# Optimization experiments

Measured on AMD Instinct MI355X. Metric: run time of the kernel, lower is better.

Reference implementation:

```python
import jax, jax.numpy as jnp
import numpy as np

SMOOTH = 1.0

def reference(probs, targets):
    B = probs.shape[0]
    m1 = probs.reshape(B, -1)
    m2 = targets.reshape(B, -1)
    # thresholded prediction and per-sample argmax ground truth (original acc branch)
    SR = m1 > 0.5
    GT = m2 == jnp.max(m2, axis=1, keepdims=True)
    corr = jnp.sum(SR == GT, axis=1).astype(jnp.float32)
    # original divides by SR.shape[0] == probs.shape[1] (per-sample first dim)
    acc = corr / jnp.float32(probs.shape[1])
    intersection = jnp.sum(m1 * m2, axis=1)
    score = 2.0 * (intersection + SMOOTH) / (jnp.sum(m1, axis=1) + jnp.sum(m2, axis=1) + SMOOTH)
    score = jnp.where(acc == 1.0, jnp.float32(1.0), score)
    return jnp.mean(1.0 - score)

def setup_inputs() -> dict:
    key = jax.random.key(0)
    k1, k2 = jax.random.split(key)
    probs = jax.random.uniform(k1, (32, 1, 512, 512), dtype=jnp.float32)
    targets = jax.random.uniform(k2, (32, 1, 512, 512), dtype=jnp.float32)
    return {"probs": probs, "targets": targets}
```

## Files before the change

kernel.cpp:

```cpp
#include <hip/hip_runtime.h>
#include <math.h>

#define NS 32
#define NELEM 262144
#define TPB 256

__device__ __forceinline__ unsigned f2u(float x) { return __builtin_bit_cast(unsigned, x); }
__device__ __forceinline__ float u2f(unsigned x) { return __builtin_bit_cast(float, x); }

__device__ __forceinline__ void comb(float& mx, int& pk, float m2, int pk2) {
    const bool g = m2 > mx;
    const bool e = m2 == mx;
    pk = g ? pk2 : (pk + (e ? pk2 : 0));
    mx = fmaxf(mx, m2);
}

template<int CTRL>
__device__ __forceinline__ float dppf(float v) {
    return u2f((unsigned)__builtin_amdgcn_update_dpp((int)f2u(v), (int)f2u(v),
                                                     CTRL, 0xF, 0xF, false));
}
template<int CTRL>
__device__ __forceinline__ int dppi(int v) {
    return __builtin_amdgcn_update_dpp(v, v, CTRL, 0xF, 0xF, false);
}

template<int N>
__device__ __forceinline__ void level_ror(float& s1, float& s2, float& dt,
                                          int& cgt, float& mx, int& pk) {
    s1 += dppf<0x120 + N>(s1);
    s2 += dppf<0x120 + N>(s2);
    dt += dppf<0x120 + N>(dt);
    cgt += dppi<0x120 + N>(cgt);
    const float m2 = dppf<0x120 + N>(mx);
    const int   p2 = dppi<0x120 + N>(pk);
    comb(mx, pk, m2, p2);
}

#if __has_builtin(__builtin_amdgcn_permlane16_swap) && __has_builtin(__builtin_amdgcn_permlane32_swap)
template<bool WIDE>
__device__ __forceinline__ void level_swap(float& s1, float& s2, float& dt,
                                           int& cgt, float& mx, int& pk) {
#define SWAP_(x) (WIDE ? __builtin_amdgcn_permlane32_swap((x), (x), false, false) \
                       : __builtin_amdgcn_permlane16_swap((x), (x), false, false))
    { auto r = SWAP_(f2u(s1)); s1 = u2f(r[0]) + u2f(r[1]); }
    { auto r = SWAP_(f2u(s2)); s2 = u2f(r[0]) + u2f(r[1]); }
    { auto r = SWAP_(f2u(dt)); dt = u2f(r[0]) + u2f(r[1]); }
    { auto r = SWAP_((unsigned)cgt); cgt = (int)(r[0] + r[1]); }
    { auto rm = SWAP_(f2u(mx));
      auto rp = SWAP_((unsigned)pk);
      float mA = u2f(rm[0]); int pA = (int)rp[0];
      comb(mA, pA, u2f(rm[1]), (int)rp[1]);
      mx = mA; pk = pA; }
#undef SWAP_
}
#else
template<bool WIDE>
__device__ __forceinline__ void level_swap(float& s1, float& s2, float& dt,
                                           int& cgt, float& mx, int& pk) {
    const int off = WIDE ? 32 : 16;
    s1 += __shfl_xor(s1, off);
    s2 += __shfl_xor(s2, off);
    dt += __shfl_xor(dt, off);
    cgt += __shfl_xor(cgt, off);
    const float m2 = __shfl_xor(mx, off);
    const int   p2 = __shfl_xor(pk, off);
    comb(mx, pk, m2, p2);
}
#endif

template<int PASSES, int MINW>
__global__ __launch_bounds__(TPB, MINW) void k_partial(const float* __restrict__ probs,
                                                       const float* __restrict__ tgts,
                                                       float* __restrict__ wsf,
                                                       int* __restrict__ wsi,
                                                       int nsets) {
    constexpr int BPS = NELEM / (PASSES * TPB * 16);
    const int b = blockIdx.x;
    const int s = b / BPS;
    const int c = b % BPS;
    const size_t base = (size_t)s * NELEM + (size_t)c * (PASSES * TPB * 16);
    const float4* __restrict__ p4 = (const float4*)(probs + base);
    const float4* __restrict__ t4 = (const float4*)(tgts + base);
    const int t = threadIdx.x;

    float4 a1 = {0.f,0.f,0.f,0.f}, a2 = {0.f,0.f,0.f,0.f}, ad = {0.f,0.f,0.f,0.f};
    int cgt = 0, pk = 0;
    float mx = -INFINITY;

#pragma unroll
    for (int g = 0; g < PASSES; ++g) {
        float4 pv[4], tv[4];
#pragma unroll
        for (int k = 0; k < 4; ++k) {
            pv[k] = p4[g * 1024 + k * 256 + t];
            tv[k] = t4[g * 1024 + k * 256 + t];
        }
#pragma unroll
        for (int k = 0; k < 4; ++k) {
            a1.x += pv[k].x; a1.y += pv[k].y; a1.z += pv[k].z; a1.w += pv[k].w;
            a2.x += tv[k].x; a2.y += tv[k].y; a2.z += tv[k].z; a2.w += tv[k].w;
            ad.x = fmaf(pv[k].x, tv[k].x, ad.x);
            ad.y = fmaf(pv[k].y, tv[k].y, ad.y);
            ad.z = fmaf(pv[k].z, tv[k].z, ad.z);
            ad.w = fmaf(pv[k].w, tv[k].w, ad.w);
        }
        const float mX = fmaxf(fmaxf(tv[0].x, tv[1].x), fmaxf(tv[2].x, tv[3].x));
        const float mY = fmaxf(fmaxf(tv[0].y, tv[1].y), fmaxf(tv[2].y, tv[3].y));
        const float mZ = fmaxf(fmaxf(tv[0].z, tv[1].z), fmaxf(tv[2].z, tv[3].z));
        const float mW = fmaxf(fmaxf(tv[0].w, tv[1].w), fmaxf(tv[2].w, tv[3].w));
        const float mg = fmaxf(fmaxf(mX, mY), fmaxf(mZ, mW));
        int cp = 0, cg = 0, gg = 0;
#pragma unroll
        for (int k = 0; k < 4; ++k) {
            const float pc[4] = {pv[k].x, pv[k].y, pv[k].z, pv[k].w};
            const float tc[4] = {tv[k].x, tv[k].y, tv[k].z, tv[k].w};
#pragma unroll
            for (int j = 0; j < 4; ++j) {
                const int b1 = pc[j] > 0.5f;
                const int eq = tc[j] == mg;
                cp += b1;
                cg += eq;
                gg += eq & b1;
            }
        }
        cgt += cp;
        comb(mx, pk, mg, (cg << 16) | gg);
    }

    float s1 = (a1.x + a1.y) + (a1.z + a1.w);
    float s2 = (a2.x + a2.y) + (a2.z + a2.w);
    float dt = (ad.x + ad.y) + (ad.z + ad.w);

    level_ror<8>(s1, s2, dt, cgt, mx, pk);
    level_ror<4>(s1, s2, dt, cgt, mx, pk);
    level_ror<2>(s1, s2, dt, cgt, mx, pk);
    level_ror<1>(s1, s2, dt, cgt, mx, pk);
    level_swap<false>(s1, s2, dt, cgt, mx, pk);
    level_swap<true >(s1, s2, dt, cgt, mx, pk);

    if ((t & 63) == 0) {
        const int g = b * (TPB / 64) + (t >> 6);
        wsf[0 * nsets + g] = s1;
        wsf[1 * nsets + g] = s2;
        wsf[2 * nsets + g] = dt;
        wsf[3 * nsets + g] = mx;
        wsi[4 * nsets + g] = cgt;
        wsi[5 * nsets + g] = pk;
    }
}

__device__ __forceinline__ void combine_max(float& mx, int& cnt, int& gt,
                                            float mx2, int cnt2, int gt2) {
    if (mx2 > mx) { mx = mx2; cnt = cnt2; gt = gt2; }
    else if (mx2 == mx) { cnt += cnt2; gt += gt2; }
}

template<int SPS>
__global__ __launch_bounds__(SPS) void k_sample(const float* __restrict__ wsf,
                                                const int* __restrict__ wsi,
                                                float* __restrict__ scores,
                                                int nsets) {
    const int s = blockIdx.x;
    const int t = threadIdx.x;
    const int idx = s * SPS + t;

    float s1 = wsf[0 * nsets + idx];
    float s2 = wsf[1 * nsets + idx];
    float dt = wsf[2 * nsets + idx];
    float mx = wsf[3 * nsets + idx];
    int  cgt = wsi[4 * nsets + idx];
    const int pk = wsi[5 * nsets + idx];
    int cnt = pk >> 16;
    int gt  = pk & 0xFFFF;

#pragma unroll
    for (int off = 32; off; off >>= 1) {
        s1  += __shfl_xor(s1, off);
        s2  += __shfl_xor(s2, off);
        dt  += __shfl_xor(dt, off);
        cgt += __shfl_xor(cgt, off);
        float m2 = __shfl_xor(mx, off);
        int   c2 = __shfl_xor(cnt, off);
        int   g2 = __shfl_xor(gt, off);
        combine_max(mx, cnt, gt, m2, c2, g2);
    }

    if constexpr (SPS > 64) {
        __shared__ float ls1[SPS / 64], ls2[SPS / 64], ldt[SPS / 64], lmx[SPS / 64];
        __shared__ int   lcg[SPS / 64], lcn[SPS / 64], lgt[SPS / 64];
        const int w = t >> 6;
        if ((t & 63) == 0) {
            ls1[w] = s1; ls2[w] = s2; ldt[w] = dt; lmx[w] = mx;
            lcg[w] = cgt; lcn[w] = cnt; lgt[w] = gt;
        }
        __syncthreads();
        if (t == 0) {
#pragma unroll
            for (int w2 = 1; w2 < SPS / 64; ++w2) {
                s1 += ls1[w2]; s2 += ls2[w2]; dt += ldt[w2]; cgt += lcg[w2];
                combine_max(mx, cnt, gt, lmx[w2], lcn[w2], lgt[w2]);
            }
        }
    }

    if (t == 0) {
        const int cle = NELEM - cgt;
        const long long corr = (long long)cle - (long long)cnt + 2LL * (long long)gt;
        float score = 2.0f * (dt + 1.0f) / (s1 + s2 + 1.0f);
        if (corr == 1) score = 1.0f;
        scores[s] = 1.0f - score;
    }
}

__global__ __launch_bounds__(64) void k_mean(const float* __restrict__ scores,
                                             float* __restrict__ out) {
    const int t = threadIdx.x;
    float v = (t < NS) ? scores[t] : 0.0f;
#pragma unroll
    for (int off = 32; off; off >>= 1) v += __shfl_xor(v, off);
    if (t == 0) out[0] = v * (1.0f / (float)NS);
}

extern "C" void kernel_launch(void* const* d_in, const int* in_sizes, int n_in,
                              void* d_out, int out_size, void* d_ws, size_t ws_size,
                              hipStream_t stream) {
    const float* probs = (const float*)d_in[0];
    const float* tgts  = (const float*)d_in[1];
    float* wsf = (float*)d_ws;
    int*   wsi = (int*)d_ws;
    float* out = (float*)d_out;

    const size_t need_big = (size_t)(6 * 8192 + NS) * sizeof(float);
    if (ws_size >= need_big) {
        const int nsets = 8192;
        k_partial<1, 8><<<2048, TPB, 0, stream>>>(probs, tgts, wsf, wsi, nsets);
        k_sample<256><<<NS, 256, 0, stream>>>(wsf, wsi, wsf + 6 * nsets, nsets);
        k_mean<<<1, 64, 0, stream>>>(wsf + 6 * nsets, out);
    } else {
        const int nsets = 2048;
        k_partial<4, 4><<<512, TPB, 0, stream>>>(probs, tgts, wsf, wsi, nsets);
        k_sample<64><<<NS, 64, 0, stream>>>(wsf, wsi, wsf + 6 * nsets, nsets);
        k_mean<<<1, 64, 0, stream>>>(wsf + 6 * nsets, out);
    }
}
```

Measured before the change: 20.13 us.

## Merge per-sample and mean kernels into one block and use fixed 512-block partial grid

Replaces the separate per-sample reduction and mean kernels with a single 1024-thread kernel that reduces all 32 samples and averages them through shared memory, cutting one kernel launch. The partial kernel always uses 512 blocks with four passes, kept as a runtime loop with unroll 1, instead of the 2048-block single-pass variant that was used when the workspace was large enough. This lowers launch count and finalize work, but gives fewer blocks and less memory-level parallelism in the main streaming pass.

After: 22.35 us. 1.11x slower.

```diff
diff --git a/kernel.cpp b/kernel.cpp
--- a/kernel.cpp
+++ b/kernel.cpp
@@ -4,6 +4,9 @@
 #define NS 32
 #define NELEM 262144
 #define TPB 256
+#define GRID 512
+#define CHUNK (NELEM / 16)
+#define NSETS 2048
 
 __device__ __forceinline__ unsigned f2u(float x) { return __builtin_bit_cast(unsigned, x); }
 __device__ __forceinline__ float u2f(unsigned x) { return __builtin_bit_cast(float, x); }
@@ -69,17 +72,14 @@
 }
 #endif
 
-template<int PASSES, int MINW>
-__global__ __launch_bounds__(TPB, MINW) void k_partial(const float* __restrict__ probs,
-                                                       const float* __restrict__ tgts,
-                                                       float* __restrict__ wsf,
-                                                       int* __restrict__ wsi,
-                                                       int nsets) {
-    constexpr int BPS = NELEM / (PASSES * TPB * 16);
+__global__ __launch_bounds__(TPB) void k_partial(const float* __restrict__ probs,
+                                                 const float* __restrict__ tgts,
+                                                 float* __restrict__ wsf,
+                                                 int* __restrict__ wsi) {
     const int b = blockIdx.x;
-    const int s = b / BPS;
-    const int c = b % BPS;
-    const size_t base = (size_t)s * NELEM + (size_t)c * (PASSES * TPB * 16);
+    const int s = b >> 4;
+    const int c = b & 15;
+    const size_t base = (size_t)s * NELEM + (size_t)c * CHUNK;
     const float4* __restrict__ p4 = (const float4*)(probs + base);
     const float4* __restrict__ t4 = (const float4*)(tgts + base);
     const int t = threadIdx.x;
@@ -88,8 +88,8 @@
     int cgt = 0, pk = 0;
     float mx = -INFINITY;
 
-#pragma unroll
-    for (int g = 0; g < PASSES; ++g) {
+#pragma unroll 1
+    for (int g = 0; g < 4; ++g) {
         float4 pv[4], tv[4];
 #pragma unroll
         for (int k = 0; k < 4; ++k) {
@@ -141,12 +141,12 @@
 
     if ((t & 63) == 0) {
         const int g = b * (TPB / 64) + (t >> 6);
-        wsf[0 * nsets + g] = s1;
-        wsf[1 * nsets + g] = s2;
-        wsf[2 * nsets + g] = dt;
-        wsf[3 * nsets + g] = mx;
-        wsi[4 * nsets + g] = cgt;
-        wsi[5 * nsets + g] = pk;
+        wsf[0 * NSETS + g] = s1;
+        wsf[1 * NSETS + g] = s2;
+        wsf[2 * NSETS + g] = dt;
+        wsf[3 * NSETS + g] = mx;
+        wsi[4 * NSETS + g] = cgt;
+        wsi[5 * NSETS + g] = pk;
     }
 }
 
@@ -156,70 +156,55 @@
     else if (mx2 == mx) { cnt += cnt2; gt += gt2; }
 }
 
-template<int SPS>
-__global__ __launch_bounds__(SPS) void k_sample(const float* __restrict__ wsf,
+__global__ __launch_bounds__(1024) void k_final(const float* __restrict__ wsf,
                                                 const int* __restrict__ wsi,
-                                                float* __restrict__ scores,
-                                                int nsets) {
-    const int s = blockIdx.x;
+                                                float* __restrict__ out) {
+    __shared__ float scores[NS];
     const int t = threadIdx.x;
-    const int idx = s * SPS + t;
-
-    float s1 = wsf[0 * nsets + idx];
-    float s2 = wsf[1 * nsets + idx];
-    float dt = wsf[2 * nsets + idx];
-    float mx = wsf[3 * nsets + idx];
-    int  cgt = wsi[4 * nsets + idx];
-    const int pk = wsi[5 * nsets + idx];
-    int cnt = pk >> 16;
-    int gt  = pk & 0xFFFF;
-
-#pragma unroll
-    for (int off = 32; off; off >>= 1) {
-        s1  += __shfl_xor(s1, off);
-        s2  += __shfl_xor(s2, off);
-        dt  += __shfl_xor(dt, off);
-        cgt += __shfl_xor(cgt, off);
-        float m2 = __shfl_xor(mx, off);
-        int   c2 = __shfl_xor(cnt, off);
-        int   g2 = __shfl_xor(gt, off);
-        combine_max(mx, cnt, gt, m2, c2, g2);
-    }
-
-    if constexpr (SPS > 64) {
-        __shared__ float ls1[SPS / 64], ls2[SPS / 64], ldt[SPS / 64], lmx[SPS / 64];
-        __shared__ int   lcg[SPS / 64], lcn[SPS / 64], lgt[SPS / 64];
-        const int w = t >> 6;
-        if ((t & 63) == 0) {
-            ls1[w] = s1; ls2[w] = s2; ldt[w] = dt; lmx[w] = mx;
-            lcg[w] = cgt; lcn[w] = cnt; lgt[w] = gt;
-        }
-        __syncthreads();
-        if (t == 0) {
-#pragma unroll
-            for (int w2 = 1; w2 < SPS / 64; ++w2) {
-                s1 += ls1[w2]; s2 += ls2[w2]; dt += ldt[w2]; cgt += lcg[w2];
-                combine_max(mx, cnt, gt, lmx[w2], lcn[w2], lgt[w2]);
-            }
-        }
-    }
-
-    if (t == 0) {
-        const int cle = NELEM - cgt;
-        const long long corr = (long long)cle - (long long)cnt + 2LL * (long long)gt;
-        float score = 2.0f * (dt + 1.0f) / (s1 + s2 + 1.0f);
-        if (corr == 1) score = 1.0f;
-        scores[s] = 1.0f - score;
-    }
-}
-
-__global__ __launch_bounds__(64) void k_mean(const float* __restrict__ scores,
-                                             float* __restrict__ out) {
-    const int t = threadIdx.x;
-    float v = (t < NS) ? scores[t] : 0.0f;
-#pragma unroll
-    for (int off = 32; off; off >>= 1) v += __shfl_xor(v, off);
-    if (t == 0) out[0] = v * (1.0f / (float)NS);
+    const int w = t >> 6, lane = t & 63;
+
+#pragma unroll
+    for (int r = 0; r < 2; ++r) {
+        const int samp = w * 2 + r;
+        const int idx = samp * 64 + lane;
+
+        float s1  = wsf[0 * NSETS + idx];
+        float s2  = wsf[1 * NSETS + idx];
+        float dot = wsf[2 * NSETS + idx];
+        float mx  = wsf[3 * NSETS + idx];
+        int   cgt = wsi[4 * NSETS + idx];
+        const int pk = wsi[5 * NSETS + idx];
+        int   cnt = pk >> 16;
+        int   gt  = pk & 0xFFFF;
+
+#pragma unroll
+        for (int off = 32; off; off >>= 1) {
+            s1  += __shfl_xor(s1, off);
+            s2  += __shfl_xor(s2, off);
+            dot += __shfl_xor(dot, off);
+            cgt += __shfl_xor(cgt, off);
+            float m2 = __shfl_xor(mx, off);
+            int   c2 = __shfl_xor(cnt, off);
+            int   g2 = __shfl_xor(gt, off);
+            combine_max(mx, cnt, gt, m2, c2, g2);
+        }
+
+        if (lane == 0) {
+            const int cle = NELEM - cgt;
+            const long long corr = (long long)cle - (long long)cnt + 2LL * (long long)gt;
+            float score = 2.0f * (dot + 1.0f) / (s1 + s2 + 1.0f);
+            if (corr == 1) score = 1.0f;
+            scores[samp] = 1.0f - score;
+        }
+    }
+
+    __syncthreads();
+    if (t < 64) {
+        float v = (t < NS) ? scores[t] : 0.0f;
+#pragma unroll
+        for (int off = 32; off; off >>= 1) v += __shfl_xor(v, off);
+        if (t == 0) out[0] = v * (1.0f / (float)NS);
+    }
 }
 
 extern "C" void kernel_launch(void* const* d_in, const int* in_sizes, int n_in,
@@ -231,16 +216,6 @@
     int*   wsi = (int*)d_ws;
     float* out = (float*)d_out;
 
-    const size_t need_big = (size_t)(6 * 8192 + NS) * sizeof(float);
-    if (ws_size >= need_big) {
-        const int nsets = 8192;
-        k_partial<1, 8><<<2048, TPB, 0, stream>>>(probs, tgts, wsf, wsi, nsets);
-        k_sample<256><<<NS, 256, 0, stream>>>(wsf, wsi, wsf + 6 * nsets, nsets);
-        k_mean<<<1, 64, 0, stream>>>(wsf + 6 * nsets, out);
-    } else {
-        const int nsets = 2048;
-        k_partial<4, 4><<<512, TPB, 0, stream>>>(probs, tgts, wsf, wsi, nsets);
-        k_sample<64><<<NS, 64, 0, stream>>>(wsf, wsi, wsf + 6 * nsets, nsets);
-        k_mean<<<1, 64, 0, stream>>>(wsf + 6 * nsets, out);
-    }
-}
+    k_partial<<<GRID, TPB, 0, stream>>>(probs, tgts, wsf, wsi);
+    k_final<<<1, 1024, 0, stream>>>(wsf, wsi, out);
+}
```
